# Optimization experiments

Hardware: AMD Instinct MI355X
Metric: run time of the kernel (lower is better)

## Reference

```python
import jax, jax.numpy as jnp
import numpy as np

R = 4          # args.search_range
D = 2 * R + 1  # window size per axis -> D*D = 81 output channels


def setup_inputs() -> dict:
    key = jax.random.key(0)
    k1, k2 = jax.random.split(key)
    B, C, H, W = 4, 128, 64, 128
    src = jax.random.normal(k1, (B, C, H, W), dtype=jnp.float32)
    tgt = jax.random.normal(k2, (B, C, H, W), dtype=jnp.float32)
    return {"src": src, "tgt": tgt}


def reference(src, tgt):
    # Faithful to the torch code: tgt is zero-padded by R on each spatial side,
    # then for output pixel (i, j) the window indices into the PADDED tensor are
    # I in [i-R, i+R], J in [j-R, j+R]. For i < R the index is negative, which in
    # torch wraps around -> reproduce with modular indexing.
    B, C, H, W = src.shape
    tp = jnp.pad(tgt, ((0, 0), (0, 0), (R, R), (R, R)))  # [B,C,H+2R,W+2R]
    Hp, Wp = H + 2 * R, W + 2 * R
    # col_idx[dj, j] = (j - R + dj) mod Wp
    col_idx = (jnp.arange(W)[None, :] - R + jnp.arange(D)[:, None]) % Wp  # [D,W]
    outs = []
    for di in range(D):  # small fixed loop over 9 row offsets
        row_idx = (jnp.arange(H) - R + di) % Hp        # [H]
        t_rows = tp[:, :, row_idx, :]                  # [B,C,H,Wp]
        t_win = t_rows[:, :, :, col_idx]               # [B,C,H,D,W]
        # channel-dot-product per pixel and per column offset
        outs.append(jnp.einsum('bchdw,bchw->bdhw', t_win, src))
    # channel ordering k = di*D + dj matches the original double loop over (I, J)
    return jnp.concatenate(outs, axis=1)  # [B, D*D, H, W]
```

## Files before the change

kernel.cpp:

```cpp
#include <hip/hip_runtime.h>
#include <stdint.h>

#define NB 4
#define NC 128
#define NH 64
#define NW 128
#define HW (NH * NW)
#define ND 9
#define NOUT (ND * ND)

__global__ __launch_bounds__(64) void costvol_kernel(const float* __restrict__ src,
                                                     const float* __restrict__ tgt,
                                                     float* __restrict__ out) {
  const int lane = threadIdx.x;
  const int slice = blockIdx.x >> 5;
  const int di = slice % ND;
  const int b  = slice / ND;
  const int h  = ((blockIdx.x & 31) << 1) + (lane >> 5);
  const int w0 = (lane & 31) << 2;
  const int y  = h + di - 8;

  float acc[ND][4];
#pragma unroll
  for (int dj = 0; dj < ND; ++dj)
#pragma unroll
    for (int k = 0; k < 4; ++k) acc[dj][k] = 0.0f;

  const bool q0 = (w0 - 8) >= 0;
  const bool q1 = (w0 - 4) >= 0;

  if (y >= 0) {
    const float* sp = src + (size_t)((b * NC) * NH + h) * NW + w0;
    const float* tp = tgt + (size_t)((b * NC) * NH + y) * NW;

#pragma unroll 4
    for (int c = 0; c < NC; ++c) {
      const float* spc = sp + (size_t)c * HW;
      const float* tpc = tp + (size_t)c * HW;

      const float4 sv = *(const float4*)spc;

      float t[12];
      {
        float4 t0, t1, t2;
        if (q0) t0 = *(const float4*)(tpc + w0 - 8);
        else    t0 = make_float4(0.f, 0.f, 0.f, 0.f);
        if (q1) t1 = *(const float4*)(tpc + w0 - 4);
        else    t1 = make_float4(0.f, 0.f, 0.f, 0.f);
        t2 = *(const float4*)(tpc + w0);
        t[0] = t0.x; t[1] = t0.y; t[2]  = t0.z; t[3]  = t0.w;
        t[4] = t1.x; t[5] = t1.y; t[6]  = t1.z; t[7]  = t1.w;
        t[8] = t2.x; t[9] = t2.y; t[10] = t2.z; t[11] = t2.w;
      }

#pragma unroll
      for (int dj = 0; dj < ND; ++dj) {
        acc[dj][0] = fmaf(sv.x, t[dj + 0], acc[dj][0]);
        acc[dj][1] = fmaf(sv.y, t[dj + 1], acc[dj][1]);
        acc[dj][2] = fmaf(sv.z, t[dj + 2], acc[dj][2]);
        acc[dj][3] = fmaf(sv.w, t[dj + 3], acc[dj][3]);
      }
    }
  }

#pragma unroll
  for (int dj = 0; dj < ND; ++dj) {
    float4 o;
    o.x = acc[dj][0]; o.y = acc[dj][1]; o.z = acc[dj][2]; o.w = acc[dj][3];
    *(float4*)(out + (size_t)(((b * NOUT + di * ND + dj) * NH + h) * NW + w0)) = o;
  }
}

extern "C" void kernel_launch(void* const* d_in, const int* in_sizes, int n_in,
                              void* d_out, int out_size, void* d_ws, size_t ws_size,
                              hipStream_t stream) {
  const float* src = (const float*)d_in[0];
  const float* tgt = (const float*)d_in[1];
  float* out = (float*)d_out;
  costvol_kernel<<<dim3(NB * ND * 32), dim3(64), 0, stream>>>(src, tgt, out);
}
```

Measured before the change: 99.72 us.

## Split channel reduction across four waves and combine partial sums in LDS

Each block now runs four 64-lane waves, and each wave accumulates a 32-channel slice of the 128-channel dot product. Partial sums go to shared memory and are combined after a barrier before the output store. The aim is four times more waves in flight, since the original grid of 1152 single-wave blocks leaves the GPU underoccupied and latency-bound on its serial 128-channel loop. The cost is LDS traffic, a block-wide sync and a changed order of float summation.

```diff
diff --git a/kernel.cpp b/kernel.cpp
--- a/kernel.cpp
+++ b/kernel.cpp
@@ -8,15 +8,19 @@
 #define HW (NH * NW)
 #define ND 9
 #define NOUT (ND * ND)
+#define CPW 32
 
-__global__ __launch_bounds__(64) void costvol_kernel(const float* __restrict__ src,
-                                                     const float* __restrict__ tgt,
-                                                     float* __restrict__ out) {
-  const int lane = threadIdx.x;
+__global__ __launch_bounds__(256, 4) void costvol_kernel(const float* __restrict__ src,
+                                                         const float* __restrict__ tgt,
+                                                         float* __restrict__ out) {
+  const int tid  = threadIdx.x;
+  const int lane = tid & 63;
+  const int wave = tid >> 6;
   const int slice = blockIdx.x >> 5;
   const int di = slice % ND;
   const int b  = slice / ND;
-  const int h  = ((blockIdx.x & 31) << 1) + (lane >> 5);
+  const int hp = blockIdx.x & 31;
+  const int h  = (hp << 1) + (lane >> 5);
   const int w0 = (lane & 31) << 2;
   const int y  = h + di - 8;
 
@@ -26,18 +30,15 @@
 #pragma unroll
     for (int k = 0; k < 4; ++k) acc[dj][k] = 0.0f;
 
-  const bool q0 = (w0 - 8) >= 0;
-  const bool q1 = (w0 - 4) >= 0;
+  const bool q0 = w0 >= 8;
+  const bool q1 = w0 >= 4;
 
   if (y >= 0) {
-    const float* sp = src + (size_t)((b * NC) * NH + h) * NW + w0;
-    const float* tp = tgt + (size_t)((b * NC) * NH + y) * NW;
+    const float* spc = src + (size_t)((b * NC + wave * CPW) * NH + h) * NW + w0;
+    const float* tpc = tgt + (size_t)((b * NC + wave * CPW) * NH + y) * NW;
 
 #pragma unroll 4
-    for (int c = 0; c < NC; ++c) {
-      const float* spc = sp + (size_t)c * HW;
-      const float* tpc = tp + (size_t)c * HW;
-
+    for (int c = 0; c < CPW; ++c) {
       const float4 sv = *(const float4*)spc;
 
       float t[12];
@@ -60,14 +61,36 @@
         acc[dj][2] = fmaf(sv.z, t[dj + 2], acc[dj][2]);
         acc[dj][3] = fmaf(sv.w, t[dj + 3], acc[dj][3]);
       }
+
+      spc += HW;
+      tpc += HW;
     }
   }
 
+  __shared__ float lds[4][ND][64][4];
 #pragma unroll
   for (int dj = 0; dj < ND; ++dj) {
+    float4 v;
+    v.x = acc[dj][0]; v.y = acc[dj][1]; v.z = acc[dj][2]; v.w = acc[dj][3];
+    *(float4*)&lds[wave][dj][lane][0] = v;
+  }
+  __syncthreads();
+
+  for (int s = tid; s < ND * 64; s += 256) {
+    const int dj = s >> 6;
+    const int l  = s & 63;
+    const float4 r0 = *(const float4*)&lds[0][dj][l][0];
+    const float4 r1 = *(const float4*)&lds[1][dj][l][0];
+    const float4 r2 = *(const float4*)&lds[2][dj][l][0];
+    const float4 r3 = *(const float4*)&lds[3][dj][l][0];
     float4 o;
-    o.x = acc[dj][0]; o.y = acc[dj][1]; o.z = acc[dj][2]; o.w = acc[dj][3];
-    *(float4*)(out + (size_t)(((b * NOUT + di * ND + dj) * NH + h) * NW + w0)) = o;
+    o.x = (r0.x + r1.x) + (r2.x + r3.x);
+    o.y = (r0.y + r1.y) + (r2.y + r3.y);
+    o.z = (r0.z + r1.z) + (r2.z + r3.z);
+    o.w = (r0.w + r1.w) + (r2.w + r3.w);
+    const int hh = (hp << 1) + (l >> 5);
+    const int ww = (l & 31) << 2;
+    *(float4*)(out + (size_t)(((b * NOUT + di * ND + dj) * NH + hh) * NW + ww)) = o;
   }
 }
 
@@ -77,5 +100,5 @@
   const float* src = (const float*)d_in[0];
   const float* tgt = (const float*)d_in[1];
   float* out = (float*)d_out;
-  costvol_kernel<<<dim3(NB * ND * 32), dim3(64), 0, stream>>>(src, tgt, out);
+  costvol_kernel<<<dim3(NB * ND * 32), dim3(256), 0, stream>>>(src, tgt, out);
 }
```

After: 93.43 us. 6.3% less time.

## Tile cost volume spatially with LDS-staged, double-buffered channel chunks

Applied to the files above, without the earlier changes.

Each block now handles an 8x16 spatial tile for all nine row offsets. It stages tgt (with halo) and src for 8 channels at a time in shared memory, and register-prefetches the next chunk while the current one is computed. This is meant to remove the ninefold redundant global reads of tgt and src across row offsets in the old per-(b,di) grid. In exchange the grid is small: 256 blocks of 320 threads, with 64 threads partly idle. There is also a barrier per chunk and only one block per CU, so latency hiding is limited.

```diff
diff --git a/kernel.cpp b/kernel.cpp
--- a/kernel.cpp
+++ b/kernel.cpp
@@ -5,20 +5,35 @@
 #define NC 128
 #define NH 64
 #define NW 128
-#define HW (NH * NW)
 #define ND 9
 #define NOUT (ND * ND)
 
-__global__ __launch_bounds__(64) void costvol_kernel(const float* __restrict__ src,
-                                                     const float* __restrict__ tgt,
-                                                     float* __restrict__ out) {
-  const int lane = threadIdx.x;
-  const int slice = blockIdx.x >> 5;
-  const int di = slice % ND;
-  const int b  = slice / ND;
-  const int h  = ((blockIdx.x & 31) << 1) + (lane >> 5);
-  const int w0 = (lane & 31) << 2;
-  const int y  = h + di - 8;
+#define TH 8
+#define TW 16
+#define CCH 8
+#define NCHUNK (NC / CCH)
+#define TGT_F4 768
+#define SRC_F4 256
+#define SRC_OFF 3072
+#define BUF_F 4096
+
+__global__ __launch_bounds__(320, 1)
+void costvol_kernel(const float* __restrict__ src,
+                    const float* __restrict__ tgt,
+                    float* __restrict__ out) {
+  __shared__ float lds[2][BUF_F];
+
+  const int tid = threadIdx.x;
+  const int bid = blockIdx.x;
+  const int b  = bid >> 6;
+  const int tile = bid & 63;
+  const int h0 = (tile >> 3) * TH;
+  const int w0 = (tile & 7) * TW;
+
+  const int di = tid >> 5;
+  const int q  = tid & 31;
+  const int r  = q >> 2;
+  const int qc = q & 3;
 
   float acc[ND][4];
 #pragma unroll
@@ -26,48 +41,89 @@
 #pragma unroll
     for (int k = 0; k < 4; ++k) acc[dj][k] = 0.0f;
 
-  const bool q0 = (w0 - 8) >= 0;
-  const bool q1 = (w0 - 4) >= 0;
+  float4 treg[3];
+  float4 sreg;
 
-  if (y >= 0) {
-    const float* sp = src + (size_t)((b * NC) * NH + h) * NW + w0;
-    const float* tp = tgt + (size_t)((b * NC) * NH + y) * NW;
+  auto load_regs = [&](int chunk) {
+    const int c0 = chunk * CCH;
+#pragma unroll
+    for (int j = 0; j < 3; ++j) {
+      const int i = tid + j * 320;
+      if (i < TGT_F4) {
+        const int ch = i / 96;
+        const int rem = i - ch * 96;
+        const int row = rem / 6;
+        const int cq = rem - row * 6;
+        const int y = h0 - 8 + row;
+        const int x = w0 - 8 + 4 * cq;
+        if (y >= 0 && x >= 0) {
+          treg[j] = *(const float4*)(tgt + (size_t)(((b * NC + c0 + ch) * NH + y) * NW + x));
+        } else {
+          treg[j] = make_float4(0.f, 0.f, 0.f, 0.f);
+        }
+      }
+    }
+    if (tid < SRC_F4) {
+      const int ch = tid >> 5;
+      const int rem = tid & 31;
+      const int row = rem >> 2;
+      const int cq = rem & 3;
+      sreg = *(const float4*)(src + (size_t)(((b * NC + c0 + ch) * NH + h0 + row) * NW + w0 + 4 * cq));
+    }
+  };
 
-#pragma unroll 4
-    for (int c = 0; c < NC; ++c) {
-      const float* spc = sp + (size_t)c * HW;
-      const float* tpc = tp + (size_t)c * HW;
+  auto write_lds = [&](int buf) {
+#pragma unroll
+    for (int j = 0; j < 3; ++j) {
+      const int i = tid + j * 320;
+      if (i < TGT_F4) *(float4*)&lds[buf][4 * i] = treg[j];
+    }
+    if (tid < SRC_F4) *(float4*)&lds[buf][SRC_OFF + 4 * tid] = sreg;
+  };
 
-      const float4 sv = *(const float4*)spc;
+  load_regs(0);
+  write_lds(0);
+  int cur = 0;
 
-      float t[12];
-      {
-        float4 t0, t1, t2;
-        if (q0) t0 = *(const float4*)(tpc + w0 - 8);
-        else    t0 = make_float4(0.f, 0.f, 0.f, 0.f);
-        if (q1) t1 = *(const float4*)(tpc + w0 - 4);
-        else    t1 = make_float4(0.f, 0.f, 0.f, 0.f);
-        t2 = *(const float4*)(tpc + w0);
+  for (int k = 0; k < NCHUNK; ++k) {
+    if (k + 1 < NCHUNK) load_regs(k + 1);
+    __syncthreads();
+
+    if (di < ND) {
+      const float* sb = &lds[cur][SRC_OFF + r * TW + 4 * qc];
+      const float* tb = &lds[cur][(r + di) * 24 + 4 * qc];
+#pragma unroll
+      for (int ch = 0; ch < CCH; ++ch) {
+        const float4 sv = *(const float4*)(sb + ch * (TH * TW));
+        const float* tp = tb + ch * 384;
+        const float4 t0 = *(const float4*)(tp);
+        const float4 t1 = *(const float4*)(tp + 4);
+        const float4 t2 = *(const float4*)(tp + 8);
+        float t[12];
         t[0] = t0.x; t[1] = t0.y; t[2]  = t0.z; t[3]  = t0.w;
         t[4] = t1.x; t[5] = t1.y; t[6]  = t1.z; t[7]  = t1.w;
         t[8] = t2.x; t[9] = t2.y; t[10] = t2.z; t[11] = t2.w;
-      }
-
 #pragma unroll
-      for (int dj = 0; dj < ND; ++dj) {
-        acc[dj][0] = fmaf(sv.x, t[dj + 0], acc[dj][0]);
-        acc[dj][1] = fmaf(sv.y, t[dj + 1], acc[dj][1]);
-        acc[dj][2] = fmaf(sv.z, t[dj + 2], acc[dj][2]);
-        acc[dj][3] = fmaf(sv.w, t[dj + 3], acc[dj][3]);
+        for (int dj = 0; dj < ND; ++dj) {
+          acc[dj][0] = fmaf(sv.x, t[dj + 0], acc[dj][0]);
+          acc[dj][1] = fmaf(sv.y, t[dj + 1], acc[dj][1]);
+          acc[dj][2] = fmaf(sv.z, t[dj + 2], acc[dj][2]);
+          acc[dj][3] = fmaf(sv.w, t[dj + 3], acc[dj][3]);
+        }
       }
     }
+
+    if (k + 1 < NCHUNK) write_lds(cur ^ 1);
+    cur ^= 1;
   }
 
+  if (di < ND) {
 #pragma unroll
-  for (int dj = 0; dj < ND; ++dj) {
-    float4 o;
-    o.x = acc[dj][0]; o.y = acc[dj][1]; o.z = acc[dj][2]; o.w = acc[dj][3];
-    *(float4*)(out + (size_t)(((b * NOUT + di * ND + dj) * NH + h) * NW + w0)) = o;
+    for (int dj = 0; dj < ND; ++dj) {
+      float4 o;
+      o.x = acc[dj][0]; o.y = acc[dj][1]; o.z = acc[dj][2]; o.w = acc[dj][3];
+      *(float4*)(out + (size_t)(((b * NOUT + di * ND + dj) * NH + h0 + r) * NW + w0 + 4 * qc)) = o;
+    }
   }
 }
 
@@ -77,5 +133,5 @@
   const float* src = (const float*)d_in[0];
   const float* tgt = (const float*)d_in[1];
   float* out = (float*)d_out;
-  costvol_kernel<<<dim3(NB * ND * 32), dim3(64), 0, stream>>>(src, tgt, out);
+  costvol_kernel<<<dim3(NB * (NH / TH) * (NW / TW)), dim3(320), 0, stream>>>(src, tgt, out);
 }
```

Result: slower. 105.2 us (+5.5%).

## Split channel reduction across blocks and reuse target rows across three di offsets

Applied to the files above, without the earlier changes.

Replaces the single kernel with a two-stage scheme. Stage one splits the 128 channels into four quarters across blocks, and each thread loads one target row and reuses it against three source rows, covering three row offsets at once. Partial sums go to a workspace buffer, and a second kernel adds the four quarters and writes zeros for invalid rows. This is meant to fix low occupancy (the original launched only 1152 single-wave blocks) and to cut redundant target loads. The cost is a large workspace round-trip of four times the output size, plus an extra launch.

```diff
diff --git a/kernel.cpp b/kernel.cpp
--- a/kernel.cpp
+++ b/kernel.cpp
@@ -7,11 +7,127 @@
 #define NW 128
 #define HW (NH * NW)
 #define ND 9
-#define NOUT (ND * ND)
+#define NOUT 81
+#define NQ 4
+#define CQ 32
+#define QS (NB * NOUT * HW)
 
-__global__ __launch_bounds__(64) void costvol_kernel(const float* __restrict__ src,
-                                                     const float* __restrict__ tgt,
-                                                     float* __restrict__ out) {
+__global__ __launch_bounds__(192)
+void costvol_stage1(const float* __restrict__ src,
+                    const float* __restrict__ tgt,
+                    float* __restrict__ ws) {
+  const int tid  = threadIdx.x;
+  const int s    = tid >> 6;
+  const int lane = tid & 63;
+  const int bid  = blockIdx.x;
+  const int bc   = bid & 15;
+  const int b    = bc >> 2;
+  const int cq   = bc & 3;
+  const int y    = ((bid >> 4) << 1) + (lane >> 5);
+  const int wq   = lane & 31;
+  const int w0   = wq << 2;
+  const int h0   = y + 3 * s;
+
+  const bool q0 = (wq >= 2);
+  const bool q1 = (wq >= 1);
+  const int ct0 = q0 ? (w0 - 8) : 0;
+  const int ct1 = q1 ? (w0 - 4) : 0;
+
+  const int r0 = (h0 + 0 < NH) ? (h0 + 0) : 0;
+  const int r1 = (h0 + 1 < NH) ? (h0 + 1) : 0;
+  const int r2 = (h0 + 2 < NH) ? (h0 + 2) : 0;
+
+  const size_t base = (size_t)(b * NC + cq * CQ) * HW;
+  const float* tp  = tgt + base + (size_t)y  * NW;
+  const float* sp0 = src + base + (size_t)r0 * NW + w0;
+  const float* sp1 = src + base + (size_t)r1 * NW + w0;
+  const float* sp2 = src + base + (size_t)r2 * NW + w0;
+
+  float acc[3][ND][4];
+#pragma unroll
+  for (int j = 0; j < 3; ++j)
+#pragma unroll
+    for (int dj = 0; dj < ND; ++dj)
+#pragma unroll
+      for (int p = 0; p < 4; ++p) acc[j][dj][p] = 0.0f;
+
+#pragma unroll 2
+  for (int c = 0; c < CQ; ++c) {
+    float4 t0 = *(const float4*)(tp + ct0);
+    float4 t1 = *(const float4*)(tp + ct1);
+    const float4 t2 = *(const float4*)(tp + w0);
+    const float4 s0 = *(const float4*)sp0;
+    const float4 s1 = *(const float4*)sp1;
+    const float4 s2 = *(const float4*)sp2;
+    if (!q0) { t0.x = 0.f; t0.y = 0.f; t0.z = 0.f; t0.w = 0.f; }
+    if (!q1) { t1.x = 0.f; t1.y = 0.f; t1.z = 0.f; t1.w = 0.f; }
+
+    float T[12];
+    T[0] = t0.x; T[1] = t0.y; T[2]  = t0.z; T[3]  = t0.w;
+    T[4] = t1.x; T[5] = t1.y; T[6]  = t1.z; T[7]  = t1.w;
+    T[8] = t2.x; T[9] = t2.y; T[10] = t2.z; T[11] = t2.w;
+    const float S0[4] = {s0.x, s0.y, s0.z, s0.w};
+    const float S1[4] = {s1.x, s1.y, s1.z, s1.w};
+    const float S2[4] = {s2.x, s2.y, s2.z, s2.w};
+
+#pragma unroll
+    for (int dj = 0; dj < ND; ++dj) {
+#pragma unroll
+      for (int p = 0; p < 4; ++p) {
+        acc[0][dj][p] = fmaf(S0[p], T[p + dj], acc[0][dj][p]);
+        acc[1][dj][p] = fmaf(S1[p], T[p + dj], acc[1][dj][p]);
+        acc[2][dj][p] = fmaf(S2[p], T[p + dj], acc[2][dj][p]);
+      }
+    }
+
+    tp += HW; sp0 += HW; sp1 += HW; sp2 += HW;
+  }
+
+  const int dibase = 8 - 3 * s;
+#pragma unroll
+  for (int j = 0; j < 3; ++j) {
+    const int h = h0 + j;
+    if (h < NH) {
+      const int di = dibase - j;
+      float* op = ws + (size_t)cq * QS
+                + (size_t)((b * NOUT + di * ND) * NH + h) * NW + w0;
+#pragma unroll
+      for (int dj = 0; dj < ND; ++dj) {
+        float4 o;
+        o.x = acc[j][dj][0]; o.y = acc[j][dj][1];
+        o.z = acc[j][dj][2]; o.w = acc[j][dj][3];
+        *(float4*)(op + (size_t)dj * HW) = o;
+      }
+    }
+  }
+}
+
+__global__ __launch_bounds__(256)
+void costvol_stage2(const float* __restrict__ ws, float* __restrict__ out) {
+  const int i4 = blockIdx.x * 256 + threadIdx.x;
+  const size_t i = (size_t)i4 * 4;
+  const int h   = (i4 >> 5) & 63;
+  const int t   = i4 >> 11;
+  const int c81 = t % 81;
+  const int di  = c81 / 9;
+  float4 o = make_float4(0.f, 0.f, 0.f, 0.f);
+  if (h + di >= 8) {
+    const float4 a = *(const float4*)(ws + i);
+    const float4 b4 = *(const float4*)(ws + (size_t)QS + i);
+    const float4 c4 = *(const float4*)(ws + (size_t)2 * QS + i);
+    const float4 d4 = *(const float4*)(ws + (size_t)3 * QS + i);
+    o.x = (a.x + b4.x) + (c4.x + d4.x);
+    o.y = (a.y + b4.y) + (c4.y + d4.y);
+    o.z = (a.z + b4.z) + (c4.z + d4.z);
+    o.w = (a.w + b4.w) + (c4.w + d4.w);
+  }
+  *(float4*)(out + i) = o;
+}
+
+__global__ __launch_bounds__(64)
+void costvol_fallback(const float* __restrict__ src,
+                      const float* __restrict__ tgt,
+                      float* __restrict__ out) {
   const int lane = threadIdx.x;
   const int slice = blockIdx.x >> 5;
   const int di = slice % ND;
@@ -26,33 +142,22 @@
 #pragma unroll
     for (int k = 0; k < 4; ++k) acc[dj][k] = 0.0f;
 
-  const bool q0 = (w0 - 8) >= 0;
-  const bool q1 = (w0 - 4) >= 0;
+  const bool q0 = w0 >= 8;
+  const bool q1 = w0 >= 4;
 
   if (y >= 0) {
-    const float* sp = src + (size_t)((b * NC) * NH + h) * NW + w0;
-    const float* tp = tgt + (size_t)((b * NC) * NH + y) * NW;
-
+    const float* spc = src + (size_t)((b * NC) * NH + h) * NW + w0;
+    const float* tpc = tgt + (size_t)((b * NC) * NH + y) * NW;
 #pragma unroll 4
     for (int c = 0; c < NC; ++c) {
-      const float* spc = sp + (size_t)c * HW;
-      const float* tpc = tp + (size_t)c * HW;
-
       const float4 sv = *(const float4*)spc;
-
       float t[12];
-      {
-        float4 t0, t1, t2;
-        if (q0) t0 = *(const float4*)(tpc + w0 - 8);
-        else    t0 = make_float4(0.f, 0.f, 0.f, 0.f);
-        if (q1) t1 = *(const float4*)(tpc + w0 - 4);
-        else    t1 = make_float4(0.f, 0.f, 0.f, 0.f);
-        t2 = *(const float4*)(tpc + w0);
-        t[0] = t0.x; t[1] = t0.y; t[2]  = t0.z; t[3]  = t0.w;
-        t[4] = t1.x; t[5] = t1.y; t[6]  = t1.z; t[7]  = t1.w;
-        t[8] = t2.x; t[9] = t2.y; t[10] = t2.z; t[11] = t2.w;
-      }
-
+      float4 t0 = q0 ? *(const float4*)(tpc + w0 - 8) : make_float4(0.f, 0.f, 0.f, 0.f);
+      float4 t1 = q1 ? *(const float4*)(tpc + w0 - 4) : make_float4(0.f, 0.f, 0.f, 0.f);
+      float4 t2 = *(const float4*)(tpc + w0);
+      t[0] = t0.x; t[1] = t0.y; t[2]  = t0.z; t[3]  = t0.w;
+      t[4] = t1.x; t[5] = t1.y; t[6]  = t1.z; t[7]  = t1.w;
+      t[8] = t2.x; t[9] = t2.y; t[10] = t2.z; t[11] = t2.w;
 #pragma unroll
       for (int dj = 0; dj < ND; ++dj) {
         acc[dj][0] = fmaf(sv.x, t[dj + 0], acc[dj][0]);
@@ -60,9 +165,10 @@
         acc[dj][2] = fmaf(sv.z, t[dj + 2], acc[dj][2]);
         acc[dj][3] = fmaf(sv.w, t[dj + 3], acc[dj][3]);
       }
+      spc += HW;
+      tpc += HW;
     }
   }
-
 #pragma unroll
   for (int dj = 0; dj < ND; ++dj) {
     float4 o;
@@ -77,5 +183,11 @@
   const float* src = (const float*)d_in[0];
   const float* tgt = (const float*)d_in[1];
   float* out = (float*)d_out;
-  costvol_kernel<<<dim3(NB * ND * 32), dim3(64), 0, stream>>>(src, tgt, out);
+  if (ws_size >= (size_t)NQ * QS * sizeof(float)) {
+    float* ws = (float*)d_ws;
+    costvol_stage1<<<dim3(512), dim3(192), 0, stream>>>(src, tgt, ws);
+    costvol_stage2<<<dim3(QS / 1024), dim3(256), 0, stream>>>(ws, out);
+  } else {
+    costvol_fallback<<<dim3(NB * ND * 32), dim3(64), 0, stream>>>(src, tgt, out);
+  }
 }
```

After: 105.3 us. +5.6%, slower.
